# Optimization experiments

Measured on AMD Instinct MI355X. Metric: run time of the kernel, lower is better.

The kernel has to match this reference:

```python
import jax, jax.numpy as jnp
import numpy as np

N, E, DIM, H, T, R = 50000, 400000, 128, 8, 4, 6
D = DIM // H  # head dim = 16


def setup_inputs() -> dict:
    key = jax.random.key(0)
    ks = jax.random.split(key, 12)
    s = 0.1
    return {
        "x": jax.random.normal(ks[0], (N, DIM), jnp.float32),
        "src": jax.random.randint(ks[1], (E,), 0, N),
        "dst": jax.random.randint(ks[2], (E,), 0, N),
        "ntype": jax.random.randint(ks[3], (N,), 0, T),
        "etype": jax.random.randint(ks[4], (E,), 0, R),
        # TypedLinear weights: [num_types, in, out] (no bias in DGL TypedLinear)
        "Wk": jax.random.normal(ks[5], (T, DIM, DIM), jnp.float32) * s,
        "Wq": jax.random.normal(ks[6], (T, DIM, DIM), jnp.float32) * s,
        "Wv": jax.random.normal(ks[7], (T, DIM, DIM), jnp.float32) * s,
        "Wa": jax.random.normal(ks[8], (T, DIM, DIM), jnp.float32) * s,
        # relation_pri[h][r], relation_att/msg: per-head per-etype [D,D]
        "rel_pri": jnp.ones((H, R), jnp.float32) + jax.random.normal(ks[9], (H, R), jnp.float32) * 0.1,
        "rel_att": jax.random.normal(ks[10], (H, R, D, D), jnp.float32) * 0.25,
        "rel_msg": jax.random.normal(ks[11], (H, R, D, D), jnp.float32) * 0.25,
        "skip": jnp.ones((T,), jnp.float32),  # sigmoid-gated skip per node type
        "ln_gamma": jnp.ones((DIM,), jnp.float32),
        "ln_beta": jnp.zeros((DIM,), jnp.float32),
    }


def _typed_linear(x, W, types):
    # x: [N, in], W: [Ttypes, in, out], types: [N] -> y_i = x_i @ W[types_i]
    out = jnp.zeros((x.shape[0], W.shape[-1]), x.dtype)
    for t in range(W.shape[0]):
        out = jnp.where((types == t)[:, None], x @ W[t], out)
    return out


def _typed_rel(xe, W, etype):
    # xe: [E, H, D], W: [H, Rtypes, D, D] -> y_e[h] = xe_e[h] @ W[h, etype_e]
    out = jnp.zeros_like(xe)
    for r in range(W.shape[1]):
        yr = jnp.einsum('ehd,hdo->eho', xe, W[:, r])
        out = jnp.where((etype == r)[:, None, None], yr, out)
    return out


def reference(x, src, dst, ntype, etype, Wk, Wq, Wv, Wa, rel_pri, rel_att, rel_msg, skip, ln_gamma, ln_beta):
    # ---- HGTConv ----
    k = _typed_linear(x, Wk, ntype).reshape(N, H, D)
    q = _typed_linear(x, Wq, ntype).reshape(N, H, D)
    v = _typed_linear(x, Wv, ntype).reshape(N, H, D)
    k_e = k[src]   # [E,H,D]
    q_e = q[dst]
    v_e = v[src]
    kw = _typed_rel(k_e, rel_att, etype)                       # [E,H,D]
    a = (kw * q_e).sum(-1) * rel_pri.T[etype] / jnp.sqrt(jnp.float32(D))  # [E,H]
    m = _typed_rel(v_e, rel_msg, etype)                        # [E,H,D]
    # edge softmax over incoming edges per dst node, per head
    amax = jax.lax.stop_gradient(jax.ops.segment_max(a, dst, num_segments=N))
    amax = jnp.where(jnp.isfinite(amax), amax, 0.0)
    ex = jnp.exp(a - amax[dst])
    den = jax.ops.segment_sum(ex, dst, num_segments=N)
    attn = ex / jnp.maximum(den[dst], 1e-9)                    # [E,H]
    h = jax.ops.segment_sum(m * attn[:, :, None], dst, num_segments=N).reshape(N, DIM)
    h = _typed_linear(h, Wa, ntype)  # dropout = identity (eval mode)
    gate = jax.nn.sigmoid(skip)[ntype][:, None]
    h = h * gate + x * (1.0 - gate)  # in_dim == out_dim -> identity skip path
    # ---- RelationAwareLayer tail: Identity residual + dropout(identity) + LayerNorm ----
    y = x + h
    mu = y.mean(-1, keepdims=True)
    var = ((y - mu) ** 2).mean(-1, keepdims=True)
    return (y - mu) / jnp.sqrt(var + 1e-5) * ln_gamma + ln_beta
```

## Files before the change

kernel.cpp:

```cpp
#include <hip/hip_runtime.h>
#include <math.h>

#define N_NODES 50000
#define N_EDGES 400000
#define H_HEADS 8
#define D_HEAD 16
#define R_TYPES 6
#define T_TYPES 4
#define DIM 128
#define BN 16
#define MAX_TILES ((N_NODES + BN - 1) / BN + T_TYPES)
#define NKEYS (N_NODES * R_TYPES)
#define NBLK_K ((NKEYS + 255) / 256)
#define NBLK_N ((N_NODES + 255) / 256)
#define EPAD_ALIGN 128
#define EPAD_MAX (N_EDGES + R_TYPES * EPAD_ALIGN)
#define SM_SHIFT 8.0f

typedef unsigned short bf16_t;

__device__ __forceinline__ float bf2f(bf16_t u) {
    unsigned int v = ((unsigned int)u) << 16;
    return __int_as_float((int)v);
}
__device__ __forceinline__ bf16_t f2bf(float f) {
    unsigned int u = (unsigned int)__float_as_int(f);
    unsigned int lsb = (u >> 16) & 1u;
    u += 0x7fffu + lsb;
    return (bf16_t)(u >> 16);
}
__device__ __forceinline__ void bf2x(unsigned int u, float& a, float& b) {
    a = bf2f((bf16_t)(u & 0xffffu));
    b = bf2f((bf16_t)(u >> 16));
}
__device__ __forceinline__ unsigned int pk(float a, float b) {
    return (unsigned int)f2bf(a) | ((unsigned int)f2bf(b) << 16);
}


__global__ void k_scanA(const int* __restrict__ cnt, int* __restrict__ offs,
                        int* __restrict__ partial, int n) {
    __shared__ int tmp[256];
    int tid = threadIdx.x;
    int i = blockIdx.x * 256 + tid;
    int v = (i < n) ? cnt[i] : 0;
    tmp[tid] = v;
    __syncthreads();
    for (int o = 1; o < 256; o <<= 1) {
        int t = (tid >= o) ? tmp[tid - o] : 0;
        __syncthreads();
        tmp[tid] += t;
        __syncthreads();
    }
    if (i < n) offs[i] = tmp[tid] - v;
    if (tid == 255) partial[blockIdx.x] = tmp[255];
}

__device__ void dev_rscan(int* a, int total, int* tmp, int* carry_s) {
    int tid = threadIdx.x;
    if (tid == 0) *carry_s = 0;
    __syncthreads();
    for (int base = 0; base < total; base += 256) {
        int i = base + tid;
        int v = (i < total) ? a[i] : 0;
        tmp[tid] = v;
        __syncthreads();
        for (int o = 1; o < 256; o <<= 1) {
            int t = (tid >= o) ? tmp[tid - o] : 0;
            __syncthreads();
            tmp[tid] += t;
            __syncthreads();
        }
        int carry = *carry_s;
        if (i < total) a[i] = carry + tmp[tid] - v;
        __syncthreads();
        if (tid == 255) *carry_s = carry + tmp[255];
        __syncthreads();
    }
}

__global__ void k_rscan2(int* __restrict__ a, int na, int* __restrict__ b, int nb) {
    __shared__ int tmp[256];
    __shared__ int carry_s;
    dev_rscan(a, na, tmp, &carry_s);
    __syncthreads();
    dev_rscan(b, nb, tmp, &carry_s);
}

__global__ void k_scanC2(int* __restrict__ offs, const int* __restrict__ partial,
                         int* __restrict__ cursor, int n) {
    int i = blockIdx.x * 256 + threadIdx.x;
    if (i < n) {
        int v = offs[i] + partial[blockIdx.x];
        offs[i] = v;
        cursor[i] = v;
    }
}


__global__ void k_count_all(const int* __restrict__ src, const int* __restrict__ dst,
                            const int* __restrict__ etype,
                            int* __restrict__ deg6, int* __restrict__ degD, int n) {
    int e = blockIdx.x * blockDim.x + threadIdx.x;
    if (e < n) {
        atomicAdd(&deg6[etype[e] * N_NODES + src[e]], 1);
        atomicAdd(&degD[dst[e]], 1);
    }
}

__global__ void k_tcount_agg(const int* __restrict__ ntype, int* __restrict__ tcnt,
                             int* __restrict__ wpos, int n) {
    __shared__ int hist[T_TYPES];
    __shared__ int base[T_TYPES];
    int tid = threadIdx.x;
    if (tid < T_TYPES) hist[tid] = 0;
    __syncthreads();
    int i = blockIdx.x * 256 + tid;
    int t = 0, rank = 0;
    if (i < n) {
        t = ntype[i];
        rank = atomicAdd(&hist[t], 1);
    }
    __syncthreads();
    if (tid < T_TYPES)
        base[tid] = (hist[tid] > 0) ? atomicAdd(&tcnt[tid], hist[tid]) : 0;
    __syncthreads();
    if (i < n) wpos[i] = base[t] + rank;
}


__global__ void k_small_setup(const int* __restrict__ offs6, const int* __restrict__ partial6,
                              const int* __restrict__ tcnt,
                              int* __restrict__ rb_pad, int* __restrict__ rstart,
                              int* __restrict__ pbase, int* __restrict__ ntiles_g,
                              int* __restrict__ tile_type, int* __restrict__ nlist,
                              int* __restrict__ esrc_s, int nE) {
    __shared__ int rbp[R_TYPES + 1], rst[R_TYPES], len[R_TYPES];
    __shared__ int off_t[T_TYPES + 1];
    int tid = threadIdx.x;
    if (tid == 0) {
        int o = 0;
        int st = offs6[0] + partial6[0];
        for (int r = 0; r < R_TYPES; ++r) {
            int idx1 = (r + 1) * N_NODES;
            int en = (r < R_TYPES - 1) ? (offs6[idx1] + partial6[idx1 >> 8]) : nE;
            rst[r] = st; rstart[r] = st;
            len[r] = en - st;
            rbp[r] = o; rb_pad[r] = o;
            o += (en - st + EPAD_ALIGN - 1) & ~(EPAD_ALIGN - 1);
            st = en;
        }
        rbp[R_TYPES] = o; rb_pad[R_TYPES] = o;
        int o2 = 0;
        for (int t = 0; t < T_TYPES; ++t) {
            off_t[t] = o2;
            pbase[t] = o2 * BN;
            o2 += (tcnt[t] + BN - 1) / BN;
        }
        off_t[T_TYPES] = o2;
        *ntiles_g = o2;
    }
    __syncthreads();
    for (int r = 0; r < R_TYPES; ++r)
        for (int i = rbp[r] + len[r] + tid; i < rbp[r + 1]; i += 256) esrc_s[i] = -1;
    for (int i = rbp[R_TYPES] + tid; i < EPAD_MAX; i += 256) esrc_s[i] = -1;
    int total = off_t[T_TYPES];
    for (int i = tid; i < total; i += 256) {
        int t = 0;
        while (t < T_TYPES - 1 && i >= off_t[t + 1]) ++t;
        tile_type[i] = t;
    }
    for (int t = 0; t < T_TYPES; ++t) {
        int b0 = off_t[t] * BN + tcnt[t];
        int b1 = off_t[t + 1] * BN;
        for (int i = b0 + tid; i < b1; i += 256) nlist[i] = -1;
    }
}

__global__ void k_cursor_pad(const int* __restrict__ offs6, const int* __restrict__ partial6,
                             const int* __restrict__ rb_pad, const int* __restrict__ rstart,
                             int* __restrict__ cursor6, int n) {
    int i = blockIdx.x * 256 + threadIdx.x;
    if (i < n) {
        int r = i / N_NODES;
        int v = offs6[i] + partial6[i >> 8];
        cursor6[i] = rb_pad[r] + (v - rstart[r]);
    }
}

__global__ void k_scatter6D(const int* __restrict__ src, const int* __restrict__ dst,
                            const int* __restrict__ etype, int* __restrict__ cursor6,
                            int* __restrict__ cursorD,
                            int* __restrict__ esrc_s, int* __restrict__ edst_s,
                            int* __restrict__ dpos, int n) {
    int e = blockIdx.x * blockDim.x + threadIdx.x;
    if (e < n) {
        int dn = dst[e];
        int key = etype[e] * N_NODES + src[e];
        int pos = atomicAdd(&cursor6[key], 1);
        esrc_s[pos] = src[e];
        edst_s[pos] = dn;
        dpos[pos] = atomicAdd(&cursorD[dn], 1);
    }
}

__global__ void k_tscatter2(const int* __restrict__ ntype, const int* __restrict__ wpos,
                            const int* __restrict__ pbase, int* __restrict__ nlist, int n) {
    int i = blockIdx.x * 256 + threadIdx.x;
    if (i < n) nlist[pbase[ntype[i]] + wpos[i]] = i;
}


__global__ __launch_bounds__(192) void k_kqv_gemm4(
    const float* __restrict__ x, const int* __restrict__ nlist,
    const int* __restrict__ tile_type, const int* __restrict__ ntiles_g,
    const float* __restrict__ Wk, const float* __restrict__ Wq,
    const float* __restrict__ Wv,
    bf16_t* __restrict__ kb, bf16_t* __restrict__ qb, bf16_t* __restrict__ vb) {
    __shared__ float xs[BN][DIM];
    __shared__ int sids[BN];
    int b = blockIdx.x;
    if (b >= *ntiles_g) return;
    int tid = threadIdx.x;
    if (tid < BN) sids[tid] = nlist[b * BN + tid];
    __syncthreads();
    for (int idx = tid; idx < BN * (DIM / 4); idx += 192) {
        int row = idx >> 5;
        int q4 = idx & 31;
        int nid = sids[row];
        float4 v4 = make_float4(0.f, 0.f, 0.f, 0.f);
        if (nid >= 0) v4 = *(const float4*)(x + (size_t)nid * DIM + q4 * 4);
        *(float4*)(&xs[row][q4 * 4]) = v4;
    }
    __syncthreads();
    int lt = tid / 96;
    int wi = tid % 96;
    int mat = wi >> 5;
    int colq = wi & 31;
    int t = tile_type[b];
    const float* W = (mat == 0 ? Wk : (mat == 1 ? Wq : Wv))
                     + (size_t)t * DIM * DIM + colq * 4;
    float acc[8][4];
#pragma unroll
    for (int n = 0; n < 8; ++n) {
        acc[n][0] = 0.f; acc[n][1] = 0.f; acc[n][2] = 0.f; acc[n][3] = 0.f;
    }
    const float* xbase = &xs[lt * 8][0];
    for (int dq = 0; dq < 32; ++dq) {
        float4 w0 = *(const float4*)(W + (size_t)(dq * 4 + 0) * DIM);
        float4 w1 = *(const float4*)(W + (size_t)(dq * 4 + 1) * DIM);
        float4 w2 = *(const float4*)(W + (size_t)(dq * 4 + 2) * DIM);
        float4 w3 = *(const float4*)(W + (size_t)(dq * 4 + 3) * DIM);
#pragma unroll
        for (int n = 0; n < 8; ++n) {
            float4 xv = *(const float4*)(xbase + n * DIM + dq * 4);
            acc[n][0] = fmaf(xv.x, w0.x, acc[n][0]);
            acc[n][0] = fmaf(xv.y, w1.x, acc[n][0]);
            acc[n][0] = fmaf(xv.z, w2.x, acc[n][0]);
            acc[n][0] = fmaf(xv.w, w3.x, acc[n][0]);
            acc[n][1] = fmaf(xv.x, w0.y, acc[n][1]);
            acc[n][1] = fmaf(xv.y, w1.y, acc[n][1]);
            acc[n][1] = fmaf(xv.z, w2.y, acc[n][1]);
            acc[n][1] = fmaf(xv.w, w3.y, acc[n][1]);
            acc[n][2] = fmaf(xv.x, w0.z, acc[n][2]);
            acc[n][2] = fmaf(xv.y, w1.z, acc[n][2]);
            acc[n][2] = fmaf(xv.z, w2.z, acc[n][2]);
            acc[n][2] = fmaf(xv.w, w3.z, acc[n][2]);
            acc[n][3] = fmaf(xv.x, w0.w, acc[n][3]);
            acc[n][3] = fmaf(xv.y, w1.w, acc[n][3]);
            acc[n][3] = fmaf(xv.z, w2.w, acc[n][3]);
            acc[n][3] = fmaf(xv.w, w3.w, acc[n][3]);
        }
    }
    bf16_t* ob = (mat == 0 ? kb : (mat == 1 ? qb : vb));
#pragma unroll
    for (int n = 0; n < 8; ++n) {
        int nid = sids[lt * 8 + n];
        if (nid >= 0) {
            ushort4 o4;
            o4.x = f2bf(acc[n][0]); o4.y = f2bf(acc[n][1]);
            o4.z = f2bf(acc[n][2]); o4.w = f2bf(acc[n][3]);
            *(ushort4*)(ob + (size_t)nid * DIM + colq * 4) = o4;
        }
    }
}


__global__ __launch_bounds__(256) void k_edge_m3(
    const bf16_t* __restrict__ kbuf, const bf16_t* __restrict__ qbuf,
    const bf16_t* __restrict__ vbuf,
    const int* __restrict__ esrc_s, const int* __restrict__ edst_s,
    const int* __restrict__ rb_pad, const int* __restrict__ dpos,
    const float* __restrict__ rel_att, const float* __restrict__ rel_msg,
    const float* __restrict__ rel_pri,
    float* __restrict__ ex_out, bf16_t* __restrict__ m_out) {
    __shared__ float A2[8 * 260];
    __shared__ float M2[8 * 260];
    __shared__ float pri[8];
    __shared__ int r_s;
    int b = blockIdx.x;
    int e0 = b * EPAD_ALIGN;
    int tid = threadIdx.x;
    if (tid == 0) {
        int r = 0;
#pragma unroll
        for (int q = 1; q < R_TYPES; ++q) if (e0 >= rb_pad[q]) r = q;
        r_s = r;
    }
    __syncthreads();
    int r = r_s;
    for (int idx = tid; idx < 2048; idx += 256) {
        int h = idx >> 8, dj = idx & 255;
        A2[h * 260 + dj] = rel_att[(h * R_TYPES + r) * 256 + dj];
        M2[h * 260 + dj] = rel_msg[(h * R_TYPES + r) * 256 + dj];
    }
    if (tid < 8) pri[tid] = rel_pri[tid * R_TYPES + r] * 0.25f;
    __syncthreads();
    int el = tid >> 3;
    int h  = tid & 7;
    const float4* A4 = (const float4*)&A2[h * 260];
    const float4* M4 = (const float4*)&M2[h * 260];
    float prih = pri[h];

    for (int it = 0; it < EPAD_ALIGN / 32; ++it) {
        int q2 = e0 + it * 32 + el;
        int s = esrc_s[q2];
        if (s < 0) continue;
        int dn = edst_s[q2];
        const uint4* kp = (const uint4*)(kbuf + (size_t)s  * DIM + h * 16);
        const uint4* qp = (const uint4*)(qbuf + (size_t)dn * DIM + h * 16);
        const uint4* vp = (const uint4*)(vbuf + (size_t)s  * DIM + h * 16);
        uint4 ka = kp[0], kb4 = kp[1];
        uint4 qa = qp[0], qb4 = qp[1];
        uint4 va = vp[0], vb4 = vp[1];
        float kk[16], qq[16], vv[16];
        bf2x(ka.x,  kk[0],  kk[1]);  bf2x(ka.y,  kk[2],  kk[3]);
        bf2x(ka.z,  kk[4],  kk[5]);  bf2x(ka.w,  kk[6],  kk[7]);
        bf2x(kb4.x, kk[8],  kk[9]);  bf2x(kb4.y, kk[10], kk[11]);
        bf2x(kb4.z, kk[12], kk[13]); bf2x(kb4.w, kk[14], kk[15]);
        bf2x(qa.x,  qq[0],  qq[1]);  bf2x(qa.y,  qq[2],  qq[3]);
        bf2x(qa.z,  qq[4],  qq[5]);  bf2x(qa.w,  qq[6],  qq[7]);
        bf2x(qb4.x, qq[8],  qq[9]);  bf2x(qb4.y, qq[10], qq[11]);
        bf2x(qb4.z, qq[12], qq[13]); bf2x(qb4.w, qq[14], qq[15]);
        bf2x(va.x,  vv[0],  vv[1]);  bf2x(va.y,  vv[2],  vv[3]);
        bf2x(va.z,  vv[4],  vv[5]);  bf2x(va.w,  vv[6],  vv[7]);
        bf2x(vb4.x, vv[8],  vv[9]);  bf2x(vb4.y, vv[10], vv[11]);
        bf2x(vb4.z, vv[12], vv[13]); bf2x(vb4.w, vv[14], vv[15]);

        float accj[16];
#pragma unroll
        for (int j = 0; j < 16; ++j) accj[j] = 0.f;
#pragma unroll
        for (int d = 0; d < 16; ++d) {
            float kd = kk[d];
#pragma unroll
            for (int jj = 0; jj < 4; ++jj) {
                float4 a4 = A4[d * 4 + jj];
                accj[jj * 4 + 0] = fmaf(kd, a4.x, accj[jj * 4 + 0]);
                accj[jj * 4 + 1] = fmaf(kd, a4.y, accj[jj * 4 + 1]);
                accj[jj * 4 + 2] = fmaf(kd, a4.z, accj[jj * 4 + 2]);
                accj[jj * 4 + 3] = fmaf(kd, a4.w, accj[jj * 4 + 3]);
            }
        }
        float a = 0.f;
#pragma unroll
        for (int j = 0; j < 16; ++j) a = fmaf(accj[j], qq[j], a);
        float ex = __expf(a * prih - SM_SHIFT);

        float mj[16];
#pragma unroll
        for (int j = 0; j < 16; ++j) mj[j] = 0.f;
#pragma unroll
        for (int d = 0; d < 16; ++d) {
            float vd = vv[d];
#pragma unroll
            for (int jj = 0; jj < 4; ++jj) {
                float4 m4 = M4[d * 4 + jj];
                mj[jj * 4 + 0] = fmaf(vd, m4.x, mj[jj * 4 + 0]);
                mj[jj * 4 + 1] = fmaf(vd, m4.y, mj[jj * 4 + 1]);
                mj[jj * 4 + 2] = fmaf(vd, m4.z, mj[jj * 4 + 2]);
                mj[jj * 4 + 3] = fmaf(vd, m4.w, mj[jj * 4 + 3]);
            }
        }
        int dp = dpos[q2];
        ex_out[(size_t)dp * 8 + h] = ex;
        uint4 o0, o1;
        o0.x = pk(ex * mj[0],  ex * mj[1]);  o0.y = pk(ex * mj[2],  ex * mj[3]);
        o0.z = pk(ex * mj[4],  ex * mj[5]);  o0.w = pk(ex * mj[6],  ex * mj[7]);
        o1.x = pk(ex * mj[8],  ex * mj[9]);  o1.y = pk(ex * mj[10], ex * mj[11]);
        o1.z = pk(ex * mj[12], ex * mj[13]); o1.w = pk(ex * mj[14], ex * mj[15]);
        uint4* op = (uint4*)(m_out + (size_t)dp * DIM + h * 16);
        op[0] = o0; op[1] = o1;
    }
}


__global__ __launch_bounds__(256) void k_agg_stream(
    const bf16_t* __restrict__ m_out, const float* __restrict__ ex_out,
    const int* __restrict__ doffD, const int* __restrict__ degD,
    float* __restrict__ hacc, int n) {
    int tid = threadIdx.x;
    int nb = tid >> 7;
    int lane2 = tid & 127;
    int node = blockIdx.x * 2 + nb;
    if (node >= n) return;
    int h = lane2 >> 4;
    int off = doffD[node];
    int dg  = degD[node];
    float acc = 0.f, den = 0.f;
#pragma unroll 4
    for (int j = 0; j < dg; ++j) {
        den += ex_out[(size_t)(off + j) * 8 + h];
        acc += bf2f(m_out[(size_t)(off + j) * DIM + lane2]);
    }
    hacc[(size_t)node * DIM + lane2] = acc / fmaxf(den, 1e-9f);
}


__global__ __launch_bounds__(256) void k_final_gemm(
    const float* __restrict__ x, const int* __restrict__ nlist,
    const int* __restrict__ tile_type, const int* __restrict__ ntiles_g,
    const float* __restrict__ Wa, const float* __restrict__ skip,
    const float* __restrict__ gamma, const float* __restrict__ beta,
    float* __restrict__ out) {
    __shared__ float hs[BN][DIM];
    __shared__ float ys[BN][DIM];
    __shared__ int sids[BN];
    __shared__ float mred[BN], ired[BN];
    int b = blockIdx.x;
    if (b >= *ntiles_g) return;
    int tid = threadIdx.x;
    if (tid < BN) sids[tid] = nlist[b * BN + tid];
    __syncthreads();
    for (int idx = tid; idx < BN * DIM; idx += 256) {
        int row = idx >> 7, col = idx & 127;
        int nid = sids[row];
        hs[row][col] = (nid >= 0) ? out[(size_t)nid * DIM + col] : 0.f;
    }
    __syncthreads();
    int t = tile_type[b];
    int half = tid >> 7, col = tid & 127;
    const float* W = Wa + (size_t)t * DIM * DIM;
    float acc[8];
#pragma unroll
    for (int n = 0; n < 8; ++n) acc[n] = 0.f;
#pragma unroll 4
    for (int d = 0; d < DIM; ++d) {
        float w = W[d * DIM + col];
#pragma unroll
        for (int n = 0; n < 8; ++n) acc[n] = fmaf(hs[half * 8 + n][d], w, acc[n]);
    }
    float gte = 1.f / (1.f + __expf(-skip[t]));
#pragma unroll
    for (int n = 0; n < 8; ++n) {
        int row = half * 8 + n;
        int nid = sids[row];
        float xv = (nid >= 0) ? x[(size_t)nid * DIM + col] : 0.f;
        ys[row][col] = xv * (2.f - gte) + acc[n] * gte;
    }
    __syncthreads();
    int ng = tid >> 4, l16 = tid & 15;
    float s = 0.f, s2 = 0.f;
#pragma unroll
    for (int k2 = 0; k2 < 8; ++k2) {
        float yv = ys[ng][l16 + 16 * k2];
        s += yv; s2 += yv * yv;
    }
#pragma unroll
    for (int m = 1; m < 16; m <<= 1) {
        s  += __shfl_xor(s, m, 64);
        s2 += __shfl_xor(s2, m, 64);
    }
    if (l16 == 0) {
        float mu = s * (1.f / DIM);
        float var = s2 * (1.f / DIM) - mu * mu;
        mred[ng] = mu;
        ired[ng] = rsqrtf(var + 1e-5f);
    }
    __syncthreads();
    float gm = gamma[col], bt = beta[col];
#pragma unroll
    for (int n = 0; n < 8; ++n) {
        int row = half * 8 + n;
        int nid = sids[row];
        if (nid >= 0)
            out[(size_t)nid * DIM + col] = (ys[row][col] - mred[row]) * ired[row] * gm + bt;
    }
}


extern "C" void kernel_launch(void* const* d_in, const int* in_sizes, int n_in,
                              void* d_out, int out_size, void* d_ws, size_t ws_size,
                              hipStream_t stream) {
    const float* x       = (const float*)d_in[0];
    const int*   src     = (const int*)d_in[1];
    const int*   dst     = (const int*)d_in[2];
    const int*   ntype   = (const int*)d_in[3];
    const int*   etype   = (const int*)d_in[4];
    const float* Wk      = (const float*)d_in[5];
    const float* Wq      = (const float*)d_in[6];
    const float* Wv      = (const float*)d_in[7];
    const float* Wa      = (const float*)d_in[8];
    const float* rel_pri = (const float*)d_in[9];
    const float* rel_att = (const float*)d_in[10];
    const float* rel_msg = (const float*)d_in[11];
    const float* skip    = (const float*)d_in[12];
    const float* gamma   = (const float*)d_in[13];
    const float* beta    = (const float*)d_in[14];
    float* out = (float*)d_out;

    const int N = N_NODES, E = N_EDGES;

    char* ws = (char*)d_ws;
    float* ex_out = (float*)ws;
    int* deg6    = (int*)(ex_out + (size_t)E * H_HEADS);
    int* degD    = deg6 + NKEYS;
    int* tcnt    = degD + N;
    int* offs6   = tcnt + T_TYPES;
    int* partial6 = offs6 + NKEYS;
    int* doffD   = partial6 + NBLK_K;
    int* partialD = doffD + N;
    int* cursor6 = partialD + NBLK_N;
    int* cursorD = cursor6 + NKEYS;
    int* rb_pad  = cursorD + N;
    int* rstart  = rb_pad + R_TYPES + 1;
    int* dpos    = rstart + R_TYPES;
    int* esrc_s  = dpos + EPAD_MAX;
    int* edst_s  = esrc_s + EPAD_MAX;
    int* pbase   = edst_s + EPAD_MAX;
    int* ntiles  = pbase + T_TYPES;
    int* tile_type = ntiles + 1;
    int* nlist   = tile_type + MAX_TILES;
    int* wpos    = nlist + (size_t)MAX_TILES * BN;
    bf16_t* kb   = (bf16_t*)(wpos + N);
    bf16_t* qb   = kb + (size_t)N * DIM;
    bf16_t* vb   = qb + (size_t)N * DIM;
    bf16_t* m_out = vb + (size_t)N * DIM;

    const int nbE = (E + 255) / 256;

    hipMemsetAsync(deg6, 0, (size_t)(NKEYS + N + T_TYPES) * sizeof(int), stream);
    k_count_all<<<nbE, 256, 0, stream>>>(src, dst, etype, deg6, degD, E);
    k_tcount_agg<<<NBLK_N, 256, 0, stream>>>(ntype, tcnt, wpos, N);

    k_scanA<<<NBLK_K, 256, 0, stream>>>(deg6, offs6, partial6, NKEYS);
    k_scanA<<<NBLK_N, 256, 0, stream>>>(degD, doffD, partialD, N);
    k_rscan2<<<1, 256, 0, stream>>>(partial6, NBLK_K, partialD, NBLK_N);

    k_small_setup<<<1, 256, 0, stream>>>(
        offs6, partial6, tcnt, rb_pad, rstart, pbase, ntiles, tile_type,
        nlist, esrc_s, E);
    k_cursor_pad<<<NBLK_K, 256, 0, stream>>>(offs6, partial6, rb_pad, rstart, cursor6, NKEYS);
    k_scanC2<<<NBLK_N, 256, 0, stream>>>(doffD, partialD, cursorD, N);

    k_scatter6D<<<nbE, 256, 0, stream>>>(
        src, dst, etype, cursor6, cursorD, esrc_s, edst_s, dpos, E);
    k_tscatter2<<<NBLK_N, 256, 0, stream>>>(ntype, wpos, pbase, nlist, N);

    k_kqv_gemm4<<<MAX_TILES, 192, 0, stream>>>(
        x, nlist, tile_type, ntiles, Wk, Wq, Wv, kb, qb, vb);

    k_edge_m3<<<EPAD_MAX / EPAD_ALIGN, 256, 0, stream>>>(
        kb, qb, vb, esrc_s, edst_s, rb_pad, dpos,
        rel_att, rel_msg, rel_pri, ex_out, m_out);

    k_agg_stream<<<(N + 1) / 2, 256, 0, stream>>>(
        m_out, ex_out, doffD, degD, out, N);

    k_final_gemm<<<MAX_TILES, 256, 0, stream>>>(
        x, nlist, tile_type, ntiles, Wa, skip, gamma, beta, out);
}
```

Before: 371.6 us.

## Fuse setup kernels and fold edge aggregation into final typed GEMM

The preprocessing kernels are merged: degree counting with the node-type histogram, the partial-sum rescan with the small setup, the two cursor fills, and the edge and node scatters. This cuts the launch count. The per-node aggregation kernel is removed. Its work now happens inside the final GEMM tile kernel, where each of 16 threads per node does vectorized uint4 bf16 loads and writes the normalized result straight into shared memory. That avoids writing and re-reading the N×128 float intermediate in global memory, at the cost of fewer threads per node working through the edge loop.

```diff
diff --git a/kernel.cpp b/kernel.cpp
--- a/kernel.cpp
+++ b/kernel.cpp
@@ -79,72 +79,57 @@
     }
 }
 
-__global__ void k_rscan2(int* __restrict__ a, int na, int* __restrict__ b, int nb) {
+
+__global__ void k_count_combo(const int* __restrict__ src, const int* __restrict__ dst,
+                              const int* __restrict__ etype, const int* __restrict__ ntype,
+                              int* __restrict__ deg6, int* __restrict__ degD,
+                              int* __restrict__ tcnt, int* __restrict__ wpos,
+                              int nE, int nN) {
+    __shared__ int hist[T_TYPES];
+    __shared__ int base[T_TYPES];
+    int tid = threadIdx.x;
+    int i = blockIdx.x * 256 + tid;
+    if (tid < T_TYPES) hist[tid] = 0;
+    __syncthreads();
+    if (i < nE) {
+        atomicAdd(&deg6[etype[i] * N_NODES + src[i]], 1);
+        atomicAdd(&degD[dst[i]], 1);
+    }
+    int t = 0, rank = 0;
+    if (i < nN) {
+        t = ntype[i];
+        rank = atomicAdd(&hist[t], 1);
+    }
+    __syncthreads();
+    if (tid < T_TYPES)
+        base[tid] = (hist[tid] > 0) ? atomicAdd(&tcnt[tid], hist[tid]) : 0;
+    __syncthreads();
+    if (i < nN) wpos[i] = base[t] + rank;
+}
+
+
+__global__ void k_scan_small(int* __restrict__ partial6, int* __restrict__ partialD,
+                             const int* __restrict__ offs6, const int* __restrict__ tcnt,
+                             int* __restrict__ rb_pad, int* __restrict__ rstart,
+                             int* __restrict__ pbase, int* __restrict__ ntiles_g,
+                             int* __restrict__ tile_type, int* __restrict__ nlist,
+                             int* __restrict__ esrc_s, int nE) {
     __shared__ int tmp[256];
     __shared__ int carry_s;
-    dev_rscan(a, na, tmp, &carry_s);
-    __syncthreads();
-    dev_rscan(b, nb, tmp, &carry_s);
-}
-
-__global__ void k_scanC2(int* __restrict__ offs, const int* __restrict__ partial,
-                         int* __restrict__ cursor, int n) {
-    int i = blockIdx.x * 256 + threadIdx.x;
-    if (i < n) {
-        int v = offs[i] + partial[blockIdx.x];
-        offs[i] = v;
-        cursor[i] = v;
-    }
-}
-
-
-__global__ void k_count_all(const int* __restrict__ src, const int* __restrict__ dst,
-                            const int* __restrict__ etype,
-                            int* __restrict__ deg6, int* __restrict__ degD, int n) {
-    int e = blockIdx.x * blockDim.x + threadIdx.x;
-    if (e < n) {
-        atomicAdd(&deg6[etype[e] * N_NODES + src[e]], 1);
-        atomicAdd(&degD[dst[e]], 1);
-    }
-}
-
-__global__ void k_tcount_agg(const int* __restrict__ ntype, int* __restrict__ tcnt,
-                             int* __restrict__ wpos, int n) {
-    __shared__ int hist[T_TYPES];
-    __shared__ int base[T_TYPES];
-    int tid = threadIdx.x;
-    if (tid < T_TYPES) hist[tid] = 0;
-    __syncthreads();
-    int i = blockIdx.x * 256 + tid;
-    int t = 0, rank = 0;
-    if (i < n) {
-        t = ntype[i];
-        rank = atomicAdd(&hist[t], 1);
-    }
-    __syncthreads();
-    if (tid < T_TYPES)
-        base[tid] = (hist[tid] > 0) ? atomicAdd(&tcnt[tid], hist[tid]) : 0;
-    __syncthreads();
-    if (i < n) wpos[i] = base[t] + rank;
-}
-
-
-__global__ void k_small_setup(const int* __restrict__ offs6, const int* __restrict__ partial6,
-                              const int* __restrict__ tcnt,
-                              int* __restrict__ rb_pad, int* __restrict__ rstart,
-                              int* __restrict__ pbase, int* __restrict__ ntiles_g,
-                              int* __restrict__ tile_type, int* __restrict__ nlist,
-                              int* __restrict__ esrc_s, int nE) {
-    __shared__ int rbp[R_TYPES + 1], rst[R_TYPES], len[R_TYPES];
+    __shared__ int rbp[R_TYPES + 1], len[R_TYPES];
     __shared__ int off_t[T_TYPES + 1];
     int tid = threadIdx.x;
+    dev_rscan(partial6, NBLK_K, tmp, &carry_s);
+    __syncthreads();
+    dev_rscan(partialD, NBLK_N, tmp, &carry_s);
+    __syncthreads();
     if (tid == 0) {
         int o = 0;
         int st = offs6[0] + partial6[0];
         for (int r = 0; r < R_TYPES; ++r) {
             int idx1 = (r + 1) * N_NODES;
             int en = (r < R_TYPES - 1) ? (offs6[idx1] + partial6[idx1 >> 8]) : nE;
-            rst[r] = st; rstart[r] = st;
+            rstart[r] = st;
             len[r] = en - st;
             rbp[r] = o; rb_pad[r] = o;
             o += (en - st + EPAD_ALIGN - 1) & ~(EPAD_ALIGN - 1);
@@ -177,37 +162,43 @@
     }
 }
 
-__global__ void k_cursor_pad(const int* __restrict__ offs6, const int* __restrict__ partial6,
-                             const int* __restrict__ rb_pad, const int* __restrict__ rstart,
-                             int* __restrict__ cursor6, int n) {
+
+__global__ void k_cursor_combo(const int* __restrict__ offs6, const int* __restrict__ partial6,
+                               const int* __restrict__ rb_pad, const int* __restrict__ rstart,
+                               int* __restrict__ cursor6,
+                               int* __restrict__ doffD, const int* __restrict__ partialD,
+                               int* __restrict__ cursorD, int nK, int nN) {
     int i = blockIdx.x * 256 + threadIdx.x;
-    if (i < n) {
+    if (i < nK) {
         int r = i / N_NODES;
         int v = offs6[i] + partial6[i >> 8];
         cursor6[i] = rb_pad[r] + (v - rstart[r]);
     }
-}
-
-__global__ void k_scatter6D(const int* __restrict__ src, const int* __restrict__ dst,
-                            const int* __restrict__ etype, int* __restrict__ cursor6,
-                            int* __restrict__ cursorD,
-                            int* __restrict__ esrc_s, int* __restrict__ edst_s,
-                            int* __restrict__ dpos, int n) {
-    int e = blockIdx.x * blockDim.x + threadIdx.x;
-    if (e < n) {
-        int dn = dst[e];
-        int key = etype[e] * N_NODES + src[e];
+    if (i < nN) {
+        int v = doffD[i] + partialD[i >> 8];
+        doffD[i] = v;
+        cursorD[i] = v;
+    }
+}
+
+
+__global__ void k_scatter_combo(const int* __restrict__ src, const int* __restrict__ dst,
+                                const int* __restrict__ etype, const int* __restrict__ ntype,
+                                int* __restrict__ cursor6, int* __restrict__ cursorD,
+                                int* __restrict__ esrc_s, int* __restrict__ edst_s,
+                                int* __restrict__ dpos,
+                                const int* __restrict__ wpos, const int* __restrict__ pbase,
+                                int* __restrict__ nlist, int nE, int nN) {
+    int i = blockIdx.x * 256 + threadIdx.x;
+    if (i < nE) {
+        int dn = dst[i];
+        int key = etype[i] * N_NODES + src[i];
         int pos = atomicAdd(&cursor6[key], 1);
-        esrc_s[pos] = src[e];
+        esrc_s[pos] = src[i];
         edst_s[pos] = dn;
         dpos[pos] = atomicAdd(&cursorD[dn], 1);
     }
-}
-
-__global__ void k_tscatter2(const int* __restrict__ ntype, const int* __restrict__ wpos,
-                            const int* __restrict__ pbase, int* __restrict__ nlist, int n) {
-    int i = blockIdx.x * 256 + threadIdx.x;
-    if (i < n) nlist[pbase[ntype[i]] + wpos[i]] = i;
+    if (i < nN) nlist[pbase[ntype[i]] + wpos[i]] = i;
 }
 
 
@@ -395,31 +386,11 @@
 }
 
 
-__global__ __launch_bounds__(256) void k_agg_stream(
+__global__ __launch_bounds__(256) void k_final2(
+    const float* __restrict__ x, const int* __restrict__ nlist,
+    const int* __restrict__ tile_type, const int* __restrict__ ntiles_g,
     const bf16_t* __restrict__ m_out, const float* __restrict__ ex_out,
     const int* __restrict__ doffD, const int* __restrict__ degD,
-    float* __restrict__ hacc, int n) {
-    int tid = threadIdx.x;
-    int nb = tid >> 7;
-    int lane2 = tid & 127;
-    int node = blockIdx.x * 2 + nb;
-    if (node >= n) return;
-    int h = lane2 >> 4;
-    int off = doffD[node];
-    int dg  = degD[node];
-    float acc = 0.f, den = 0.f;
-#pragma unroll 4
-    for (int j = 0; j < dg; ++j) {
-        den += ex_out[(size_t)(off + j) * 8 + h];
-        acc += bf2f(m_out[(size_t)(off + j) * DIM + lane2]);
-    }
-    hacc[(size_t)node * DIM + lane2] = acc / fmaxf(den, 1e-9f);
-}
-
-
-__global__ __launch_bounds__(256) void k_final_gemm(
-    const float* __restrict__ x, const int* __restrict__ nlist,
-    const int* __restrict__ tile_type, const int* __restrict__ ntiles_g,
     const float* __restrict__ Wa, const float* __restrict__ skip,
     const float* __restrict__ gamma, const float* __restrict__ beta,
     float* __restrict__ out) {
@@ -432,10 +403,30 @@
     int tid = threadIdx.x;
     if (tid < BN) sids[tid] = nlist[b * BN + tid];
     __syncthreads();
-    for (int idx = tid; idx < BN * DIM; idx += 256) {
-        int row = idx >> 7, col = idx & 127;
+    {
+        int row = tid >> 4, d = tid & 15;
         int nid = sids[row];
-        hs[row][col] = (nid >= 0) ? out[(size_t)nid * DIM + col] : 0.f;
+        float a0=0.f,a1=0.f,a2=0.f,a3=0.f,a4=0.f,a5=0.f,a6=0.f,a7=0.f;
+        float den = 0.f;
+        if (nid >= 0) {
+            int off = doffD[nid];
+            int dg  = degD[nid];
+            int hh = d >> 1;
+#pragma unroll 2
+            for (int j = 0; j < dg; ++j) {
+                den += ex_out[(size_t)(off + j) * 8 + hh];
+                uint4 mv = *(const uint4*)(m_out + (size_t)(off + j) * DIM + d * 8);
+                float u, w;
+                bf2x(mv.x, u, w); a0 += u; a1 += w;
+                bf2x(mv.y, u, w); a2 += u; a3 += w;
+                bf2x(mv.z, u, w); a4 += u; a5 += w;
+                bf2x(mv.w, u, w); a6 += u; a7 += w;
+            }
+        }
+        float inv = 1.f / fmaxf(den, 1e-9f);
+        float* hp = &hs[row][d * 8];
+        hp[0] = a0 * inv; hp[1] = a1 * inv; hp[2] = a2 * inv; hp[3] = a3 * inv;
+        hp[4] = a4 * inv; hp[5] = a5 * inv; hp[6] = a6 * inv; hp[7] = a7 * inv;
     }
     __syncthreads();
     int t = tile_type[b];
@@ -540,22 +531,22 @@
     const int nbE = (E + 255) / 256;
 
     hipMemsetAsync(deg6, 0, (size_t)(NKEYS + N + T_TYPES) * sizeof(int), stream);
-    k_count_all<<<nbE, 256, 0, stream>>>(src, dst, etype, deg6, degD, E);
-    k_tcount_agg<<<NBLK_N, 256, 0, stream>>>(ntype, tcnt, wpos, N);
+    k_count_combo<<<nbE, 256, 0, stream>>>(
+        src, dst, etype, ntype, deg6, degD, tcnt, wpos, E, N);
 
     k_scanA<<<NBLK_K, 256, 0, stream>>>(deg6, offs6, partial6, NKEYS);
     k_scanA<<<NBLK_N, 256, 0, stream>>>(degD, doffD, partialD, N);
-    k_rscan2<<<1, 256, 0, stream>>>(partial6, NBLK_K, partialD, NBLK_N);
-
-    k_small_setup<<<1, 256, 0, stream>>>(
-        offs6, partial6, tcnt, rb_pad, rstart, pbase, ntiles, tile_type,
-        nlist, esrc_s, E);
-    k_cursor_pad<<<NBLK_K, 256, 0, stream>>>(offs6, partial6, rb_pad, rstart, cursor6, NKEYS);
-    k_scanC2<<<NBLK_N, 256, 0, stream>>>(doffD, partialD, cursorD, N);
-
-    k_scatter6D<<<nbE, 256, 0, stream>>>(
-        src, dst, etype, cursor6, cursorD, esrc_s, edst_s, dpos, E);
-    k_tscatter2<<<NBLK_N, 256, 0, stream>>>(ntype, wpos, pbase, nlist, N);
+    k_scan_small<<<1, 256, 0, stream>>>(
+        partial6, partialD, offs6, tcnt, rb_pad, rstart, pbase, ntiles,
+        tile_type, nlist, esrc_s, E);
+
+    k_cursor_combo<<<NBLK_K, 256, 0, stream>>>(
+        offs6, partial6, rb_pad, rstart, cursor6, doffD, partialD, cursorD,
+        NKEYS, N);
+
+    k_scatter_combo<<<nbE, 256, 0, stream>>>(
+        src, dst, etype, ntype, cursor6, cursorD, esrc_s, edst_s, dpos,
+        wpos, pbase, nlist, E, N);
 
     k_kqv_gemm4<<<MAX_TILES, 192, 0, stream>>>(
         x, nlist, tile_type, ntiles, Wk, Wq, Wv, kb, qb, vb);
@@ -564,9 +555,7 @@
         kb, qb, vb, esrc_s, edst_s, rb_pad, dpos,
         rel_att, rel_msg, rel_pri, ex_out, m_out);
 
-    k_agg_stream<<<(N + 1) / 2, 256, 0, stream>>>(
-        m_out, ex_out, doffD, degD, out, N);
-
-    k_final_gemm<<<MAX_TILES, 256, 0, stream>>>(
-        x, nlist, tile_type, ntiles, Wa, skip, gamma, beta, out);
-}
+    k_final2<<<MAX_TILES, 256, 0, stream>>>(
+        x, nlist, tile_type, ntiles, m_out, ex_out, doffD, degD,
+        Wa, skip, gamma, beta, out);
+}
```

Result: faster. 335.4 us (-9.7%).
